# Performance work log

Measured on AMD Instinct MI355X. Metric: run time of the kernel, lower is better.

The kernel has to match this reference:

```python
import jax, jax.numpy as jnp
import numpy as np


def setup_inputs() -> dict:
    key = jax.random.key(0)
    B, N = 16384, 4000
    f = jax.random.normal(key, (B, N), dtype=jnp.float32)
    return {"f": f, "num_stocks": N}


def reference(f, num_stocks):
    # ListMLE loss: mean_b [ -sum_i f[b,i] + sum_i logsumexp(f[b, i:]) ]
    # The original python loop recomputes logsumexp over every suffix (O(N^2));
    # this is exactly a reverse cumulative logsumexp, computed in one O(N) pass.
    rev_clse = jax.lax.cumlogsumexp(f, axis=1, reverse=True)  # [B, N]
    per_row = jnp.sum(rev_clse, axis=1) - jnp.sum(f, axis=1)  # [B]
    return jnp.mean(per_row)
```

## Files before the change

### kernel.cpp

```cpp
#include <hip/hip_runtime.h>


#define TPB 256
#define NFIX 4000
#define NVALID 250

__global__ __launch_bounds__(TPB, 8) void listmle_row_kernel(
    const float* __restrict__ f, float* __restrict__ ws) {
    __shared__ float tw[4];
    __shared__ float part[4];

    const int t    = threadIdx.x;
    const int lane = t & 63;
    const int w    = t >> 6;
    const float4* __restrict__ rf4 = (const float4*)(f + (size_t)blockIdx.x * NFIX);

    float e[16];
    float fsum = 0.f, T = 0.f;
    if (t < NVALID) {
        float4 x0 = rf4[4 * t + 0];
        float4 x1 = rf4[4 * t + 1];
        float4 x2 = rf4[4 * t + 2];
        float4 x3 = rf4[4 * t + 3];
        fsum = ((x0.x + x0.y) + (x0.z + x0.w)) + ((x1.x + x1.y) + (x1.z + x1.w))
             + ((x2.x + x2.y) + (x2.z + x2.w)) + ((x3.x + x3.y) + (x3.z + x3.w));
        e[0]  = __expf(x0.x); e[1]  = __expf(x0.y); e[2]  = __expf(x0.z); e[3]  = __expf(x0.w);
        e[4]  = __expf(x1.x); e[5]  = __expf(x1.y); e[6]  = __expf(x1.z); e[7]  = __expf(x1.w);
        e[8]  = __expf(x2.x); e[9]  = __expf(x2.y); e[10] = __expf(x2.z); e[11] = __expf(x2.w);
        e[12] = __expf(x3.x); e[13] = __expf(x3.y); e[14] = __expf(x3.z); e[15] = __expf(x3.w);
        #pragma unroll
        for (int k = 0; k < 16; ++k) T += e[k];
    } else {
        #pragma unroll
        for (int k = 0; k < 16; ++k) e[k] = 0.f;
    }

    float incl = T;
    #pragma unroll
    for (int d = 1; d < 64; d <<= 1) {
        float u = __shfl_down(incl, d, 64);
        if (lane + d < 64) incl += u;
    }
    if (lane == 0) tw[w] = incl;
    __syncthreads();

    float Rw = 0.f;
    #pragma unroll
    for (int w2 = 0; w2 < 4; ++w2) if (w2 > w) Rw += tw[w2];
    float s_run = Rw + (incl - T);

    float L = 0.f;
    if (t < NVALID) {
        #pragma unroll
        for (int k = 15; k >= 0; --k) {
            s_run += e[k];
            L += __logf(s_run);
        }
    }

    float contrib = L - fsum;
    #pragma unroll
    for (int d = 32; d > 0; d >>= 1) contrib += __shfl_down(contrib, d, 64);
    if (lane == 0) part[w] = contrib;
    __syncthreads();
    if (t == 0) ws[blockIdx.x] = (part[0] + part[1]) + (part[2] + part[3]);
}

#define RTPB 1024
__global__ __launch_bounds__(RTPB) void reduce_mean_kernel(
    const float* __restrict__ ws, float* __restrict__ out, int B) {
    __shared__ double red[RTPB / 64];
    const int t = threadIdx.x;
    const float4* __restrict__ w4 = (const float4*)ws;
    const int nv = B / 4;
    double acc = 0.0;
    for (int v = t; v < nv; v += RTPB) {
        float4 x = w4[v];
        acc += (double)x.x + (double)x.y + (double)x.z + (double)x.w;
    }
    #pragma unroll
    for (int d = 32; d > 0; d >>= 1) acc += __shfl_down(acc, d, 64);
    if ((t & 63) == 0) red[t >> 6] = acc;
    __syncthreads();
    if (t == 0) {
        double s = 0.0;
        #pragma unroll
        for (int w = 0; w < RTPB / 64; ++w) s += red[w];
        out[0] = (float)(s / (double)B);
    }
}

extern "C" void kernel_launch(void* const* d_in, const int* in_sizes, int n_in,
                              void* d_out, int out_size, void* d_ws, size_t ws_size,
                              hipStream_t stream) {
    const float* f = (const float*)d_in[0];
    const int B = in_sizes[0] / NFIX;
    float* ws = (float*)d_ws;
    float* out = (float*)d_out;

    listmle_row_kernel<<<B, TPB, 0, stream>>>(f, ws);
    reduce_mean_kernel<<<1, RTPB, 0, stream>>>(ws, out, B);
}
```

Measured before the change: 48.60 us.

## Use 512-thread blocks with 8 elements per thread and batch logs via products

Doubles threads per row so each handles 8 elements instead of 16, with block-level scan and reduction widened to 8 waves. The 16 per-element logs become two log2 calls on products of four suffix sums each, scaled by ln2. This cuts transcendental work and register pressure and shortens per-thread serial chains. The cost is a larger cross-wave reduction and some risk of overflow or underflow in the products if suffix sums get extreme.

```diff
diff --git a/kernel.cpp b/kernel.cpp
--- a/kernel.cpp
+++ b/kernel.cpp
@@ -1,38 +1,33 @@
 #include <hip/hip_runtime.h>
 
 
-#define TPB 256
+#define TPB 512
 #define NFIX 4000
-#define NVALID 250
+#define NVALID 500
+#define NROWS 16384
 
-__global__ __launch_bounds__(TPB, 8) void listmle_row_kernel(
+__global__ __launch_bounds__(TPB, 4) void listmle_row_kernel(
     const float* __restrict__ f, float* __restrict__ ws) {
-    __shared__ float tw[4];
-    __shared__ float part[4];
+    __shared__ float tw[8];
+    __shared__ float part[8];
 
     const int t    = threadIdx.x;
     const int lane = t & 63;
     const int w    = t >> 6;
     const float4* __restrict__ rf4 = (const float4*)(f + (size_t)blockIdx.x * NFIX);
 
-    float e[16];
+    float e[8];
     float fsum = 0.f, T = 0.f;
     if (t < NVALID) {
-        float4 x0 = rf4[4 * t + 0];
-        float4 x1 = rf4[4 * t + 1];
-        float4 x2 = rf4[4 * t + 2];
-        float4 x3 = rf4[4 * t + 3];
-        fsum = ((x0.x + x0.y) + (x0.z + x0.w)) + ((x1.x + x1.y) + (x1.z + x1.w))
-             + ((x2.x + x2.y) + (x2.z + x2.w)) + ((x3.x + x3.y) + (x3.z + x3.w));
-        e[0]  = __expf(x0.x); e[1]  = __expf(x0.y); e[2]  = __expf(x0.z); e[3]  = __expf(x0.w);
-        e[4]  = __expf(x1.x); e[5]  = __expf(x1.y); e[6]  = __expf(x1.z); e[7]  = __expf(x1.w);
-        e[8]  = __expf(x2.x); e[9]  = __expf(x2.y); e[10] = __expf(x2.z); e[11] = __expf(x2.w);
-        e[12] = __expf(x3.x); e[13] = __expf(x3.y); e[14] = __expf(x3.z); e[15] = __expf(x3.w);
-        #pragma unroll
-        for (int k = 0; k < 16; ++k) T += e[k];
+        float4 x0 = rf4[2 * t + 0];
+        float4 x1 = rf4[2 * t + 1];
+        fsum = ((x0.x + x0.y) + (x0.z + x0.w)) + ((x1.x + x1.y) + (x1.z + x1.w));
+        e[0] = __expf(x0.x); e[1] = __expf(x0.y); e[2] = __expf(x0.z); e[3] = __expf(x0.w);
+        e[4] = __expf(x1.x); e[5] = __expf(x1.y); e[6] = __expf(x1.z); e[7] = __expf(x1.w);
+        T = ((e[0] + e[1]) + (e[2] + e[3])) + ((e[4] + e[5]) + (e[6] + e[7]));
     } else {
         #pragma unroll
-        for (int k = 0; k < 16; ++k) e[k] = 0.f;
+        for (int k = 0; k < 8; ++k) e[k] = 0.f;
     }
 
     float incl = T;
@@ -46,16 +41,22 @@
 
     float Rw = 0.f;
     #pragma unroll
-    for (int w2 = 0; w2 < 4; ++w2) if (w2 > w) Rw += tw[w2];
+    for (int w2 = 0; w2 < 8; ++w2) if (w2 > w) Rw += tw[w2];
     float s_run = Rw + (incl - T);
 
     float L = 0.f;
     if (t < NVALID) {
-        #pragma unroll
-        for (int k = 15; k >= 0; --k) {
-            s_run += e[k];
-            L += __logf(s_run);
-        }
+        float s7 = s_run + e[7];
+        float s6 = s7 + e[6];
+        float s5 = s6 + e[5];
+        float s4 = s5 + e[4];
+        float s3 = s4 + e[3];
+        float s2 = s3 + e[2];
+        float s1 = s2 + e[1];
+        float s0 = s1 + e[0];
+        float p1 = (s7 * s6) * (s5 * s4);
+        float p0 = (s3 * s2) * (s1 * s0);
+        L = (__log2f(p1) + __log2f(p0)) * 0.6931471805599453f;
     }
 
     float contrib = L - fsum;
@@ -63,7 +64,11 @@
     for (int d = 32; d > 0; d >>= 1) contrib += __shfl_down(contrib, d, 64);
     if (lane == 0) part[w] = contrib;
     __syncthreads();
-    if (t == 0) ws[blockIdx.x] = (part[0] + part[1]) + (part[2] + part[3]);
+    if (t == 0) {
+        float s = ((part[0] + part[1]) + (part[2] + part[3]))
+                + ((part[4] + part[5]) + (part[6] + part[7]));
+        ws[blockIdx.x] = s;
+    }
 }
 
 #define RTPB 1024
```

New measurement: 44.96 us. -7.5%, faster.
